# Optimization experiments

Hardware: AMD Instinct MI355X
Metric: run time of the kernel (lower is better)

Reference implementation:

```python
import jax, jax.numpy as jnp
import numpy as np
from jax import lax

T, B, INP, HS, OUT = 256, 128, 1024, 1024, 1024


def setup_inputs() -> dict:
    key = jax.random.key(0)
    ks = jax.random.split(key, 7)
    s = 1.0 / np.sqrt(HS)  # scale params to keep tanh out of deep saturation
    return {
        "data": jax.random.normal(ks[0], (T, B, INP), jnp.float32),
        "W_ih": jax.random.normal(ks[1], (INP, HS), jnp.float32) * s,
        "W_hh": jax.random.normal(ks[2], (HS, HS), jnp.float32) * s,
        "b_i": jax.random.normal(ks[3], (HS,), jnp.float32) * s,
        "b_h": jax.random.normal(ks[4], (HS,), jnp.float32) * s,
        "W_out": jax.random.normal(ks[5], (OUT, HS), jnp.float32) * s,
        "b_out": jax.random.normal(ks[6], (OUT,), jnp.float32) * s,
    }


def reference(data, W_ih, W_hh, b_i, b_h, W_out, b_out):
    # Elman RNN: h_{t+1} = tanh(x_t @ W_ih + b_i + h_t @ W_hh + b_h)
    bias = b_i + b_h
    h0 = jnp.zeros((data.shape[1], W_hh.shape[0]), data.dtype)

    def step(h, x_t):
        h_new = jnp.tanh(x_t @ W_ih + h @ W_hh + bias)
        return h_new, None

    h_final, _ = lax.scan(step, h0, data)
    # nn.Linear: out = h @ W_out.T + b_out
    return h_final @ W_out.T + b_out
```

## Files before the change

kernel.cpp:

```cpp
#include <hip/hip_runtime.h>
#include <hip/hip_bf16.h>
#include <math.h>


typedef __attribute__((ext_vector_type(8))) short bf16x8;
typedef __attribute__((ext_vector_type(4))) float f32x4;
typedef __attribute__((ext_vector_type(4))) unsigned short u16x4;
typedef __attribute__((ext_vector_type(4))) unsigned int u32x4;
typedef __attribute__((ext_vector_type(2))) unsigned int u32x2;

#define TT 256
#define BB 128
#define HS 1024
#define H_ELEMS (BB * HS)

__device__ __forceinline__ short f2bf(float x) {
  __hip_bfloat16 b = __float2bfloat16(x);
  return *reinterpret_cast<short*>(&b);
}
__device__ __forceinline__ float bf2f(unsigned short s) {
  unsigned int u = ((unsigned int)s) << 16;
  float f;
  __builtin_memcpy(&f, &u, 4);
  return f;
}
__device__ __forceinline__ float fast_exp2(float x) {
#if __has_builtin(__builtin_amdgcn_exp2f)
  return __builtin_amdgcn_exp2f(x);
#else
  return exp2f(x);
#endif
}
__device__ __forceinline__ float fast_rcp(float x) {
#if __has_builtin(__builtin_amdgcn_rcpf)
  return __builtin_amdgcn_rcpf(x);
#else
  return 1.0f / x;
#endif
}
__device__ __forceinline__ float fast_tanh(float x) {
  float xc = fminf(fmaxf(x, -9.0f), 9.0f);
  float e = fast_exp2(2.8853900817779268f * xc);
  return (e - 1.0f) * fast_rcp(e + 1.0f);
}

__device__ __forceinline__ void mall_load_b128(u32x4* dst, const void* p) {
  asm volatile("global_load_dwordx4 %0, %1, off sc0 sc1" : "=v"(*dst) : "v"(p) : "memory");
}
__device__ __forceinline__ void mall_store_b64(void* p, u32x2 v) {
  asm volatile("global_store_dwordx2 %0, %1, off sc0 sc1" :: "v"(p), "v"(v) : "memory");
}
__device__ __forceinline__ void mall_store_b32(void* p, unsigned v) {
  asm volatile("global_store_dword %0, %1, off sc0 sc1" :: "v"(p), "v"(v) : "memory");
}
__device__ __forceinline__ unsigned mall_poll_b32(const void* p) {
  unsigned v;
  asm volatile("global_load_dword %0, %1, off sc0 sc1" : "=v"(v) : "v"(p) : "memory");
  asm volatile("s_waitcnt vmcnt(0)" : "+v"(v));
  return v;
}
__device__ __forceinline__ void wait_vm0() {
  asm volatile("s_waitcnt vmcnt(0)" ::: "memory");
}
#define TIE16(d)                                                        \
  asm volatile("s_waitcnt vmcnt(0)"                                     \
               : "+v"(d[0]), "+v"(d[1]), "+v"(d[2]), "+v"(d[3]),        \
                 "+v"(d[4]), "+v"(d[5]), "+v"(d[6]), "+v"(d[7]),        \
                 "+v"(d[8]), "+v"(d[9]), "+v"(d[10]), "+v"(d[11]),      \
                 "+v"(d[12]), "+v"(d[13]), "+v"(d[14]), "+v"(d[15]))

__global__ __launch_bounds__(256) void cvt_data(const float* __restrict__ src,
                                                __hip_bfloat16* __restrict__ dst) {
  size_t i = ((size_t)blockIdx.x * 256 + threadIdx.x) * 8;
  f32x4 a = *reinterpret_cast<const f32x4*>(src + i);
  f32x4 b = *reinterpret_cast<const f32x4*>(src + i + 4);
  bf16x8 v;
  v[0] = f2bf(a[0]); v[1] = f2bf(a[1]); v[2] = f2bf(a[2]); v[3] = f2bf(a[3]);
  v[4] = f2bf(b[0]); v[5] = f2bf(b[1]); v[6] = f2bf(b[2]); v[7] = f2bf(b[3]);
  *reinterpret_cast<bf16x8*>(dst + i) = v;
}

__global__ __launch_bounds__(256) void cvt_tr(const float* __restrict__ src,
                                              __hip_bfloat16* __restrict__ dst) {
  __shared__ __hip_bfloat16 T[64][72];
  const int tid = threadIdx.x;
  const int k0 = blockIdx.y * 64, n0 = blockIdx.x * 64;
  const int r = tid >> 4, c4 = (tid & 15) * 4;
#pragma unroll
  for (int p = 0; p < 4; ++p) {
    int kk = r + p * 16;
    f32x4 v = *reinterpret_cast<const f32x4*>(src + (size_t)(k0 + kk) * 1024 + n0 + c4);
#pragma unroll
    for (int j = 0; j < 4; ++j) T[c4 + j][kk] = __float2bfloat16(v[j]);
  }
  __syncthreads();
  const int rr = tid >> 3, u = tid & 7;
#pragma unroll
  for (int p = 0; p < 2; ++p) {
    int R = rr + p * 32;
    *reinterpret_cast<bf16x8*>(dst + (size_t)(n0 + R) * 1024 + k0 + u * 8) =
        *reinterpret_cast<const bf16x8*>(&T[R][u * 8]);
  }
}

template <bool ABF>
__global__ __launch_bounds__(256) void gemm_xw2(
    const void* __restrict__ Ain,
    const __hip_bfloat16* __restrict__ Bt,
    const float* __restrict__ b_i,
    const float* __restrict__ b_h,
    __hip_bfloat16* __restrict__ P) {
  __shared__ __hip_bfloat16 As[128][72];
  __shared__ __hip_bfloat16 Bs[128][72];

  const int tid = threadIdx.x;
  const int m0 = blockIdx.y * 128, n0 = blockIdx.x * 128;
  const int wave = tid >> 6, lane = tid & 63;
  const int wm = wave & 1, wn = wave >> 1;
  const int quad = lane >> 4, l16 = lane & 15;
  const int sr = tid >> 3, su = tid & 7;

  f32x4 acc[4][4] = {};

  for (int k0 = 0; k0 < 1024; k0 += 64) {
    __syncthreads();
#pragma unroll
    for (int p = 0; p < 4; ++p) {
      int row = sr + p * 32;
      bf16x8 av;
      if (ABF) {
        av = *reinterpret_cast<const bf16x8*>(
            (const __hip_bfloat16*)Ain + (size_t)(m0 + row) * 1024 + k0 + su * 8);
      } else {
        const float* ap = (const float*)Ain + (size_t)(m0 + row) * 1024 + k0 + su * 8;
        f32x4 x = *reinterpret_cast<const f32x4*>(ap);
        f32x4 y = *reinterpret_cast<const f32x4*>(ap + 4);
        av[0] = f2bf(x[0]); av[1] = f2bf(x[1]); av[2] = f2bf(x[2]); av[3] = f2bf(x[3]);
        av[4] = f2bf(y[0]); av[5] = f2bf(y[1]); av[6] = f2bf(y[2]); av[7] = f2bf(y[3]);
      }
      *reinterpret_cast<bf16x8*>(&As[row][su * 8]) = av;
      bf16x8 bv = *reinterpret_cast<const bf16x8*>(
          Bt + (size_t)(n0 + row) * 1024 + k0 + su * 8);
      *reinterpret_cast<bf16x8*>(&Bs[row][su * 8]) = bv;
    }
    __syncthreads();
#pragma unroll
    for (int kk = 0; kk < 2; ++kk) {
      bf16x8 af[4], bfr[4];
#pragma unroll
      for (int mi = 0; mi < 4; ++mi)
        af[mi] = *reinterpret_cast<const bf16x8*>(&As[wm * 64 + mi * 16 + l16][kk * 32 + quad * 8]);
#pragma unroll
      for (int ni = 0; ni < 4; ++ni)
        bfr[ni] = *reinterpret_cast<const bf16x8*>(&Bs[wn * 64 + ni * 16 + l16][kk * 32 + quad * 8]);
#pragma unroll
      for (int mi = 0; mi < 4; ++mi)
#pragma unroll
        for (int ni = 0; ni < 4; ++ni)
          acc[mi][ni] = __builtin_amdgcn_mfma_f32_16x16x32_bf16(af[mi], bfr[ni], acc[mi][ni], 0, 0, 0);
    }
  }

  float bias[4];
#pragma unroll
  for (int ni = 0; ni < 4; ++ni) {
    int col = n0 + wn * 64 + ni * 16 + l16;
    bias[ni] = b_i[col] + b_h[col];
  }
#pragma unroll
  for (int mi = 0; mi < 4; ++mi)
#pragma unroll
    for (int ni = 0; ni < 4; ++ni) {
      int row = m0 + wm * 64 + mi * 16 + quad * 4;
      int col = n0 + wn * 64 + ni * 16 + l16;
#pragma unroll
      for (int r = 0; r < 4; ++r)
        P[(size_t)(row + r) * 1024 + col] = __float2bfloat16(acc[mi][ni][r] + bias[ni]);
    }
}

__global__ __launch_bounds__(128) void rnn_scan5(
    const __hip_bfloat16* __restrict__ P,
    const float* __restrict__ W_hh,
    __hip_bfloat16* __restrict__ hbuf,
    unsigned* __restrict__ flags) {
  __shared__ __hip_bfloat16 Wt[32 * 1024];
  __shared__ __hip_bfloat16 Ht[16 * 1024];
  __shared__ __hip_bfloat16 Cs[16 * 36];

  const int tid = threadIdx.x;
  const int m = blockIdx.x & 7;
  const int ng = blockIdx.x >> 3;
  const int m0 = m * 16, n0 = ng * 32;

  for (int i = tid; i < 32 * 1024 / 4; i += 128) {
    int nq = i & 7, k = i >> 3;
    f32x4 v = *reinterpret_cast<const f32x4*>(W_hh + (size_t)k * 1024 + n0 + nq * 4);
#pragma unroll
    for (int j = 0; j < 4; ++j) {
      int nl = nq * 4 + j;
      int sg = (k >> 3) ^ (nl & 7);
      Wt[nl * 1024 + sg * 8 + (k & 7)] = __float2bfloat16(v[j]);
    }
  }
  __syncthreads();

  const int r8 = tid >> 3, s8 = tid & 7;
  const int w = tid >> 6, lane = tid & 63;
  const int quad = lane >> 4, l16 = lane & 15;
  const int nl = w * 16 + l16;
  const int col = n0 + nl;
  const int xorl = l16 & 7;
  const int crow = tid >> 3, cseg = tid & 7;
  unsigned* gflags = flags + m * 32;

  for (int t = 0; t < TT; ++t) {
    const __hip_bfloat16* hc = hbuf + (size_t)(t & 1) * H_ELEMS;
    __hip_bfloat16* hn = hbuf + (size_t)((t + 1) & 1) * H_ELEMS;

    const __hip_bfloat16* Pt =
        P + (size_t)t * H_ELEMS + (size_t)(m0 + quad * 4) * 1024 + col;
    unsigned short pv[4];
#pragma unroll
    for (int r = 0; r < 4; ++r)
      pv[r] = *reinterpret_cast<const unsigned short*>(Pt + (size_t)r * 1024);

    if (t > 0) {
      if (tid < 32) {
        const unsigned* fp = gflags + tid;
        int g = 0;
        while (mall_poll_b32(fp) < (unsigned)t && ++g < (1 << 18)) {}
      }
      __syncthreads();
    }

    {
      const char* src = (const char*)(hc + (size_t)(m0 + r8) * 1024) + s8 * 16;
      u32x4 d[16];
#pragma unroll
      for (int i = 0; i < 16; ++i) mall_load_b128(&d[i], src + i * 128);
      TIE16(d);
#pragma unroll
      for (int i = 0; i < 16; ++i) {
        int u = s8 + i * 8;
        int gp = u ^ (r8 & 7) ^ (u >> 4);
        *reinterpret_cast<u32x4*>(&Ht[r8 * 1024 + gp * 8]) = d[i];
      }
    }
    __syncthreads();

    f32x4 acc[4] = {{0.f, 0.f, 0.f, 0.f}, {0.f, 0.f, 0.f, 0.f},
                    {0.f, 0.f, 0.f, 0.f}, {0.f, 0.f, 0.f, 0.f}};
#pragma unroll
    for (int c = 0; c < 8; ++c) {
#pragma unroll
      for (int j = 0; j < 4; ++j) {
        int G = c * 16 + j * 4 + quad;
        int gp = G ^ xorl ^ c;
        bf16x8 af = *reinterpret_cast<const bf16x8*>(&Ht[l16 * 1024 + gp * 8]);
        int sg = G ^ (nl & 7);
        bf16x8 bfrag = *reinterpret_cast<const bf16x8*>(&Wt[nl * 1024 + sg * 8]);
        acc[j] = __builtin_amdgcn_mfma_f32_16x16x32_bf16(af, bfrag, acc[j], 0, 0, 0);
      }
    }

#pragma unroll
    for (int r = 0; r < 4; ++r) {
      float s = (acc[0][r] + acc[1][r]) + (acc[2][r] + acc[3][r]) + bf2f(pv[r]);
      Cs[(quad * 4 + r) * 36 + nl] = __float2bfloat16(fast_tanh(s));
    }
    __syncthreads();
    {
      u32x2 val = *reinterpret_cast<const u32x2*>(&Cs[crow * 36 + cseg * 4]);
      mall_store_b64(hn + (size_t)(m0 + crow) * 1024 + n0 + cseg * 4, val);
      wait_vm0();
    }
    __syncthreads();

    if (t != TT - 1 && tid == 0)
      mall_store_b32(gflags + ng, (unsigned)(t + 1));
  }
}

__global__ __launch_bounds__(256) void gemm_out(
    const __hip_bfloat16* __restrict__ h,
    const float* __restrict__ W_out,
    const float* __restrict__ b_out,
    float* __restrict__ out) {
  const int tid = threadIdx.x;
  const int wave = tid >> 6, lane = tid & 63;
  const int quad = lane >> 4, l16 = lane & 15;
  const int o = blockIdx.x * 64 + wave * 16 + l16;

  f32x4 acc[8] = {};
  for (int k0 = 0; k0 < 1024; k0 += 32) {
    f32x4 w0 = *reinterpret_cast<const f32x4*>(W_out + (size_t)o * 1024 + k0 + quad * 8);
    f32x4 w1 = *reinterpret_cast<const f32x4*>(W_out + (size_t)o * 1024 + k0 + quad * 8 + 4);
    bf16x8 bfr;
    bfr[0] = f2bf(w0[0]); bfr[1] = f2bf(w0[1]); bfr[2] = f2bf(w0[2]); bfr[3] = f2bf(w0[3]);
    bfr[4] = f2bf(w1[0]); bfr[5] = f2bf(w1[1]); bfr[6] = f2bf(w1[2]); bfr[7] = f2bf(w1[3]);
#pragma unroll
    for (int mi = 0; mi < 8; ++mi) {
      bf16x8 af = *reinterpret_cast<const bf16x8*>(h + (size_t)(mi * 16 + l16) * 1024 + k0 + quad * 8);
      acc[mi] = __builtin_amdgcn_mfma_f32_16x16x32_bf16(af, bfr, acc[mi], 0, 0, 0);
    }
  }
  const float bias = b_out[o];
#pragma unroll
  for (int mi = 0; mi < 8; ++mi)
#pragma unroll
    for (int r = 0; r < 4; ++r)
      out[(size_t)(mi * 16 + quad * 4 + r) * 1024 + o] = acc[mi][r] + bias;
}

extern "C" void kernel_launch(void* const* d_in, const int* in_sizes, int n_in,
                              void* d_out, int out_size, void* d_ws, size_t ws_size,
                              hipStream_t stream) {
  const float* data  = (const float*)d_in[0];
  const float* W_ih  = (const float*)d_in[1];
  const float* W_hh  = (const float*)d_in[2];
  const float* b_i   = (const float*)d_in[3];
  const float* b_h   = (const float*)d_in[4];
  const float* W_out = (const float*)d_in[5];
  const float* b_out = (const float*)d_in[6];
  float* out = (float*)d_out;

  char* ws = (char*)d_ws;
  const size_t OFF_P   = 0;
  const size_t OFF_H   = (size_t)TT * H_ELEMS * 2;
  const size_t OFF_FLG = OFF_H + 2 * H_ELEMS * 2;
  const size_t OFF_WT  = OFF_FLG + 1024;
  const size_t OFF_DB  = OFF_WT + 2u * 1024 * 1024;
  const size_t NEED_DB = OFF_DB + (size_t)TT * H_ELEMS * 2;

  __hip_bfloat16* P     = (__hip_bfloat16*)(ws + OFF_P);
  __hip_bfloat16* hbuf  = (__hip_bfloat16*)(ws + OFF_H);
  unsigned* flags       = (unsigned*)(ws + OFF_FLG);
  __hip_bfloat16* W_ihT = (__hip_bfloat16*)(ws + OFF_WT);
  __hip_bfloat16* dataB = (__hip_bfloat16*)(ws + OFF_DB);

  hipMemsetAsync(ws + OFF_H, 0, 2 * H_ELEMS * 2 + 1024, stream);

  cvt_tr<<<dim3(16, 16), 256, 0, stream>>>(W_ih, W_ihT);
  if (ws_size >= NEED_DB) {
    cvt_data<<<16384, 256, 0, stream>>>(data, dataB);
    gemm_xw2<true><<<dim3(8, 256), 256, 0, stream>>>(dataB, W_ihT, b_i, b_h, P);
  } else {
    gemm_xw2<false><<<dim3(8, 256), 256, 0, stream>>>(data, W_ihT, b_i, b_h, P);
  }
  rnn_scan5<<<256, 128, 0, stream>>>(P, W_hh, hbuf, flags);
  gemm_out<<<16, 256, 0, stream>>>(hbuf, W_out, b_out, out);
}
```

Measured before the change: 1.121 ms.

## Keep W_hh fragments in registers and load h directly into MFMA operands

The recurrent scan kernel now preloads each lane's 32 W_hh B-fragments into registers once, before the time loop, instead of re-reading them from LDS every step. The hidden state is loaded from global memory straight into the A-fragment register layout with 32 cache-bypassing dwordx4 loads, so the LDS staging buffer and one block barrier per step are gone. This shortens the serial critical path of each timestep. In exchange register use rises sharply (about 128 VGPRs for weights plus 128 for h), which risks spills. The per-lane global loads are also less coalesced, since each lane reads 16B at a 64B stride.

Measured after the change: 1.342 ms. 19.7% more time.

```diff
diff --git a/kernel.cpp b/kernel.cpp
--- a/kernel.cpp
+++ b/kernel.cpp
@@ -44,9 +44,6 @@
   return (e - 1.0f) * fast_rcp(e + 1.0f);
 }
 
-__device__ __forceinline__ void mall_load_b128(u32x4* dst, const void* p) {
-  asm volatile("global_load_dwordx4 %0, %1, off sc0 sc1" : "=v"(*dst) : "v"(p) : "memory");
-}
 __device__ __forceinline__ void mall_store_b64(void* p, u32x2 v) {
   asm volatile("global_store_dwordx2 %0, %1, off sc0 sc1" :: "v"(p), "v"(v) : "memory");
 }
@@ -68,6 +65,10 @@
                  "+v"(d[4]), "+v"(d[5]), "+v"(d[6]), "+v"(d[7]),        \
                  "+v"(d[8]), "+v"(d[9]), "+v"(d[10]), "+v"(d[11]),      \
                  "+v"(d[12]), "+v"(d[13]), "+v"(d[14]), "+v"(d[15]))
+
+#define ALOAD(i, OFF)                                                   \
+  asm volatile("global_load_dwordx4 %0, %1, off offset:" OFF " sc0 sc1" \
+               : "=v"(d[i]) : "v"(pa) : "memory")
 
 __global__ __launch_bounds__(256) void cvt_data(const float* __restrict__ src,
                                                 __hip_bfloat16* __restrict__ dst) {
@@ -179,13 +180,12 @@
     }
 }
 
-__global__ __launch_bounds__(128) void rnn_scan5(
+__global__ __launch_bounds__(128, 1) void rnn_scan6(
     const __hip_bfloat16* __restrict__ P,
     const float* __restrict__ W_hh,
     __hip_bfloat16* __restrict__ hbuf,
     unsigned* __restrict__ flags) {
   __shared__ __hip_bfloat16 Wt[32 * 1024];
-  __shared__ __hip_bfloat16 Ht[16 * 1024];
   __shared__ __hip_bfloat16 Cs[16 * 36];
 
   const int tid = threadIdx.x;
@@ -205,18 +205,28 @@
   }
   __syncthreads();
 
-  const int r8 = tid >> 3, s8 = tid & 7;
-  const int w = tid >> 6, lane = tid & 63;
+  const int wv = tid >> 6, lane = tid & 63;
   const int quad = lane >> 4, l16 = lane & 15;
-  const int nl = w * 16 + l16;
+  const int nl = wv * 16 + l16;
   const int col = n0 + nl;
-  const int xorl = l16 & 7;
   const int crow = tid >> 3, cseg = tid & 7;
   unsigned* gflags = flags + m * 32;
 
+  bf16x8 wreg[32];
+#pragma unroll
+  for (int wi = 0; wi < 32; ++wi) {
+    int G = wi * 4 + quad;
+    int sg = G ^ (nl & 7);
+    wreg[wi] = *reinterpret_cast<const bf16x8*>(&Wt[nl * 1024 + sg * 8]);
+  }
+
+  const size_t aoff = ((size_t)(m0 + l16) * 1024 + quad * 8) * 2;
+  const char* paA0 = (const char*)hbuf + aoff;
+  const char* paA1 = (const char*)(hbuf + H_ELEMS) + aoff;
+
   for (int t = 0; t < TT; ++t) {
-    const __hip_bfloat16* hc = hbuf + (size_t)(t & 1) * H_ELEMS;
     __hip_bfloat16* hn = hbuf + (size_t)((t + 1) & 1) * H_ELEMS;
+    const char* pa = (t & 1) ? paA1 : paA0;
 
     const __hip_bfloat16* Pt =
         P + (size_t)t * H_ELEMS + (size_t)(m0 + quad * 4) * 1024 + col;
@@ -234,20 +244,21 @@
       __syncthreads();
     }
 
+    u32x4 d[32];
+    ALOAD(0, "0");     ALOAD(1, "64");    ALOAD(2, "128");   ALOAD(3, "192");
+    ALOAD(4, "256");   ALOAD(5, "320");   ALOAD(6, "384");   ALOAD(7, "448");
+    ALOAD(8, "512");   ALOAD(9, "576");   ALOAD(10, "640");  ALOAD(11, "704");
+    ALOAD(12, "768");  ALOAD(13, "832");  ALOAD(14, "896");  ALOAD(15, "960");
+    ALOAD(16, "1024"); ALOAD(17, "1088"); ALOAD(18, "1152"); ALOAD(19, "1216");
+    ALOAD(20, "1280"); ALOAD(21, "1344"); ALOAD(22, "1408"); ALOAD(23, "1472");
+    ALOAD(24, "1536"); ALOAD(25, "1600"); ALOAD(26, "1664"); ALOAD(27, "1728");
+    ALOAD(28, "1792"); ALOAD(29, "1856"); ALOAD(30, "1920"); ALOAD(31, "1984");
     {
-      const char* src = (const char*)(hc + (size_t)(m0 + r8) * 1024) + s8 * 16;
-      u32x4 d[16];
-#pragma unroll
-      for (int i = 0; i < 16; ++i) mall_load_b128(&d[i], src + i * 128);
-      TIE16(d);
-#pragma unroll
-      for (int i = 0; i < 16; ++i) {
-        int u = s8 + i * 8;
-        int gp = u ^ (r8 & 7) ^ (u >> 4);
-        *reinterpret_cast<u32x4*>(&Ht[r8 * 1024 + gp * 8]) = d[i];
-      }
-    }
-    __syncthreads();
+      u32x4* dlo = d;
+      u32x4* dhi = d + 16;
+      TIE16(dlo);
+      TIE16(dhi);
+    }
 
     f32x4 acc[4] = {{0.f, 0.f, 0.f, 0.f}, {0.f, 0.f, 0.f, 0.f},
                     {0.f, 0.f, 0.f, 0.f}, {0.f, 0.f, 0.f, 0.f}};
@@ -255,12 +266,9 @@
     for (int c = 0; c < 8; ++c) {
 #pragma unroll
       for (int j = 0; j < 4; ++j) {
-        int G = c * 16 + j * 4 + quad;
-        int gp = G ^ xorl ^ c;
-        bf16x8 af = *reinterpret_cast<const bf16x8*>(&Ht[l16 * 1024 + gp * 8]);
-        int sg = G ^ (nl & 7);
-        bf16x8 bfrag = *reinterpret_cast<const bf16x8*>(&Wt[nl * 1024 + sg * 8]);
-        acc[j] = __builtin_amdgcn_mfma_f32_16x16x32_bf16(af, bfrag, acc[j], 0, 0, 0);
+        int wi = c * 4 + j;
+        bf16x8 af = __builtin_bit_cast(bf16x8, d[wi]);
+        acc[j] = __builtin_amdgcn_mfma_f32_16x16x32_bf16(af, wreg[wi], acc[j], 0, 0, 0);
       }
     }
 
@@ -348,6 +356,6 @@
   } else {
     gemm_xw2<false><<<dim3(8, 256), 256, 0, stream>>>(data, W_ihT, b_i, b_h, P);
   }
-  rnn_scan5<<<256, 128, 0, stream>>>(P, W_hh, hbuf, flags);
+  rnn_scan6<<<256, 128, 0, stream>>>(P, W_hh, hbuf, flags);
   gemm_out<<<16, 256, 0, stream>>>(hbuf, W_out, b_out, out);
 }
```

## Widen RNN scan blocks to 128 columns and keep W_hh fragments in registers

Applied to the files above, without the earlier changes.

Restructures the persistent recurrent scan from 256 blocks of 128 threads, each owning 32 columns, to 64 blocks of 512 threads, each owning 128 columns. Each wave now holds its W_hh B-fragments in 32 bf16x8 registers, loaded once through shared memory in four chunks, so the per-step LDS reads of weights go away. Fewer blocks means fewer flags to poll per step (8 instead of 32) and a cheaper cross-block barrier. The cost is heavy register pressure from the 32-entry fragment array, and the same hidden-state tile is now loaded by fewer, larger blocks.

New measurement: 1.148 ms. 2.4% more time.

```diff
diff --git a/kernel.cpp b/kernel.cpp
--- a/kernel.cpp
+++ b/kernel.cpp
@@ -5,7 +5,6 @@
 
 typedef __attribute__((ext_vector_type(8))) short bf16x8;
 typedef __attribute__((ext_vector_type(4))) float f32x4;
-typedef __attribute__((ext_vector_type(4))) unsigned short u16x4;
 typedef __attribute__((ext_vector_type(4))) unsigned int u32x4;
 typedef __attribute__((ext_vector_type(2))) unsigned int u32x2;
 
@@ -62,12 +61,9 @@
 __device__ __forceinline__ void wait_vm0() {
   asm volatile("s_waitcnt vmcnt(0)" ::: "memory");
 }
-#define TIE16(d)                                                        \
+#define TIE4(d)                                                         \
   asm volatile("s_waitcnt vmcnt(0)"                                     \
-               : "+v"(d[0]), "+v"(d[1]), "+v"(d[2]), "+v"(d[3]),        \
-                 "+v"(d[4]), "+v"(d[5]), "+v"(d[6]), "+v"(d[7]),        \
-                 "+v"(d[8]), "+v"(d[9]), "+v"(d[10]), "+v"(d[11]),      \
-                 "+v"(d[12]), "+v"(d[13]), "+v"(d[14]), "+v"(d[15]))
+               : "+v"(d[0]), "+v"(d[1]), "+v"(d[2]), "+v"(d[3]))
 
 __global__ __launch_bounds__(256) void cvt_data(const float* __restrict__ src,
                                                 __hip_bfloat16* __restrict__ dst) {
@@ -179,40 +175,55 @@
     }
 }
 
-__global__ __launch_bounds__(128) void rnn_scan5(
+__global__ __launch_bounds__(512, 2) void rnn_scan7(
     const __hip_bfloat16* __restrict__ P,
     const float* __restrict__ W_hh,
     __hip_bfloat16* __restrict__ hbuf,
     unsigned* __restrict__ flags) {
   __shared__ __hip_bfloat16 Wt[32 * 1024];
   __shared__ __hip_bfloat16 Ht[16 * 1024];
-  __shared__ __hip_bfloat16 Cs[16 * 36];
+  __shared__ __hip_bfloat16 Cs[16 * 132];
 
   const int tid = threadIdx.x;
   const int m = blockIdx.x & 7;
   const int ng = blockIdx.x >> 3;
-  const int m0 = m * 16, n0 = ng * 32;
-
-  for (int i = tid; i < 32 * 1024 / 4; i += 128) {
-    int nq = i & 7, k = i >> 3;
-    f32x4 v = *reinterpret_cast<const f32x4*>(W_hh + (size_t)k * 1024 + n0 + nq * 4);
-#pragma unroll
-    for (int j = 0; j < 4; ++j) {
-      int nl = nq * 4 + j;
-      int sg = (k >> 3) ^ (nl & 7);
-      Wt[nl * 1024 + sg * 8 + (k & 7)] = __float2bfloat16(v[j]);
+  const int m0 = m * 16, n0 = ng * 128;
+
+  const int wv = tid >> 6, lane = tid & 63;
+  const int quad = lane >> 4, l16 = lane & 15;
+  const int colloc = wv * 16 + l16;
+  const int col = n0 + colloc;
+  const int nl = (wv & 1) * 16 + l16;
+  const int xorl = l16 & 7;
+  const int r16 = tid >> 5;
+  const int s32 = tid & 31;
+  unsigned* gflags = flags + m * 8;
+
+  bf16x8 wreg[32];
+  for (int cch = 0; cch < 4; ++cch) {
+    if (cch) __syncthreads();
+    const int nb = n0 + cch * 32;
+    for (int i = tid; i < 32 * 1024 / 4; i += 512) {
+      int nq = i & 7, k = i >> 3;
+      f32x4 v = *reinterpret_cast<const f32x4*>(W_hh + (size_t)k * 1024 + nb + nq * 4);
+#pragma unroll
+      for (int j = 0; j < 4; ++j) {
+        int nll = nq * 4 + j;
+        int sg = (k >> 3) ^ (nll & 7);
+        Wt[nll * 1024 + sg * 8 + (k & 7)] = __float2bfloat16(v[j]);
+      }
+    }
+    __syncthreads();
+    if ((wv >> 1) == cch) {
+#pragma unroll
+      for (int wi = 0; wi < 32; ++wi) {
+        int G = wi * 4 + quad;
+        int sg = G ^ (nl & 7);
+        wreg[wi] = *reinterpret_cast<const bf16x8*>(&Wt[nl * 1024 + sg * 8]);
+      }
     }
   }
   __syncthreads();
-
-  const int r8 = tid >> 3, s8 = tid & 7;
-  const int w = tid >> 6, lane = tid & 63;
-  const int quad = lane >> 4, l16 = lane & 15;
-  const int nl = w * 16 + l16;
-  const int col = n0 + nl;
-  const int xorl = l16 & 7;
-  const int crow = tid >> 3, cseg = tid & 7;
-  unsigned* gflags = flags + m * 32;
 
   for (int t = 0; t < TT; ++t) {
     const __hip_bfloat16* hc = hbuf + (size_t)(t & 1) * H_ELEMS;
@@ -226,7 +237,7 @@
       pv[r] = *reinterpret_cast<const unsigned short*>(Pt + (size_t)r * 1024);
 
     if (t > 0) {
-      if (tid < 32) {
+      if (tid < 8) {
         const unsigned* fp = gflags + tid;
         int g = 0;
         while (mall_poll_b32(fp) < (unsigned)t && ++g < (1 << 18)) {}
@@ -235,16 +246,18 @@
     }
 
     {
-      const char* src = (const char*)(hc + (size_t)(m0 + r8) * 1024) + s8 * 16;
-      u32x4 d[16];
-#pragma unroll
-      for (int i = 0; i < 16; ++i) mall_load_b128(&d[i], src + i * 128);
-      TIE16(d);
-#pragma unroll
-      for (int i = 0; i < 16; ++i) {
-        int u = s8 + i * 8;
-        int gp = u ^ (r8 & 7) ^ (u >> 4);
-        *reinterpret_cast<u32x4*>(&Ht[r8 * 1024 + gp * 8]) = d[i];
+      const char* src = (const char*)(hc + (size_t)(m0 + r16) * 1024) + s32 * 16;
+      u32x4 d[4];
+      mall_load_b128(&d[0], src);
+      mall_load_b128(&d[1], src + 512);
+      mall_load_b128(&d[2], src + 1024);
+      mall_load_b128(&d[3], src + 1536);
+      TIE4(d);
+#pragma unroll
+      for (int i = 0; i < 4; ++i) {
+        int u = s32 + i * 32;
+        int gp = u ^ (r16 & 7) ^ (u >> 4);
+        *reinterpret_cast<u32x4*>(&Ht[r16 * 1024 + gp * 8]) = d[i];
       }
     }
     __syncthreads();
@@ -258,21 +271,19 @@
         int G = c * 16 + j * 4 + quad;
         int gp = G ^ xorl ^ c;
         bf16x8 af = *reinterpret_cast<const bf16x8*>(&Ht[l16 * 1024 + gp * 8]);
-        int sg = G ^ (nl & 7);
-        bf16x8 bfrag = *reinterpret_cast<const bf16x8*>(&Wt[nl * 1024 + sg * 8]);
-        acc[j] = __builtin_amdgcn_mfma_f32_16x16x32_bf16(af, bfrag, acc[j], 0, 0, 0);
+        acc[j] = __builtin_amdgcn_mfma_f32_16x16x32_bf16(af, wreg[c * 4 + j], acc[j], 0, 0, 0);
       }
     }
 
 #pragma unroll
     for (int r = 0; r < 4; ++r) {
       float s = (acc[0][r] + acc[1][r]) + (acc[2][r] + acc[3][r]) + bf2f(pv[r]);
-      Cs[(quad * 4 + r) * 36 + nl] = __float2bfloat16(fast_tanh(s));
+      Cs[(quad * 4 + r) * 132 + colloc] = __float2bfloat16(fast_tanh(s));
     }
     __syncthreads();
     {
-      u32x2 val = *reinterpret_cast<const u32x2*>(&Cs[crow * 36 + cseg * 4]);
-      mall_store_b64(hn + (size_t)(m0 + crow) * 1024 + n0 + cseg * 4, val);
+      u32x2 val = *reinterpret_cast<const u32x2*>(&Cs[r16 * 132 + s32 * 4]);
+      mall_store_b64(hn + (size_t)(m0 + r16) * 1024 + n0 + s32 * 4, val);
       wait_vm0();
     }
     __syncthreads();
@@ -348,6 +359,6 @@
   } else {
     gemm_xw2<false><<<dim3(8, 256), 256, 0, stream>>>(data, W_ihT, b_i, b_h, P);
   }
-  rnn_scan5<<<256, 128, 0, stream>>>(P, W_hh, hbuf, flags);
+  rnn_scan7<<<64, 512, 0, stream>>>(P, W_hh, hbuf, flags);
   gemm_out<<<16, 256, 0, stream>>>(hbuf, W_out, b_out, out);
 }
```
